# Optimization experiments

Measured on AMD Instinct MI355X. Metric: run time of the kernel, lower is better.

Reference implementation:

```python
import jax, jax.numpy as jnp
import numpy as np

B, N_PIC, C, H, W, P = 32, 4, 3, 224, 224, 16
HP = H // P  # 14
NP = HP * HP  # 196 patches
D = C * P * P  # 768 = hidden_size


def setup_inputs() -> dict:
    key = jax.random.key(0)
    ks = jax.random.split(key, 12)
    s = 0.02
    def lin(k, din, dout):
        kw, kb = jax.random.split(k)
        return (jax.random.normal(kw, (din, dout), jnp.float32) * s,
                jax.random.normal(kb, (dout,), jnp.float32) * s)
    W1, b1 = lin(ks[0], D, D)
    Wq, bq = lin(ks[1], D, D)
    Wk, bk = lin(ks[2], D, D)
    Wv, bv = lin(ks[3], D, D)
    Wo1, bo1 = lin(ks[4], D, D)
    Wo2, bo2 = lin(ks[5], D, D)
    x = jax.random.normal(ks[6], (B, N_PIC, C, H, W), jnp.float32)
    return {"x": x, "W1": W1, "b1": b1, "Wq": Wq, "bq": bq, "Wk": Wk,
            "bk": bk, "Wv": Wv, "bv": bv, "Wo1": Wo1, "bo1": bo1,
            "Wo2": Wo2, "bo2": bo2}


def reference(x, W1, b1, Wq, bq, Wk, bk, Wv, bv, Wo1, bo1, Wo2, bo2):
    b = x.shape[0]
    # patchify: matches torch unfold(3,P,P).unfold(4,P,P) + permute + view
    # -> [b, N, num_patches, C*P*P] with (C, ph, pw) ordering in last dim
    p = x.reshape(b, N_PIC, C, HP, P, HP, P)
    p = p.transpose(0, 1, 3, 5, 2, 4, 6).reshape(b, N_PIC, NP, D)
    h = p @ W1 + b1  # [b, N, S, D]
    # attention: query always from picture 0; key/value per picture (batched)
    Q = h[:, 0] @ Wq + bq          # [b, S, D]
    K = h @ Wk + bk                # [b, N, S, D]
    V = h @ Wv + bv                # [b, N, S, D]
    scale = 1.0 / jnp.sqrt(jnp.float32(D))
    scores = jnp.einsum('bsd,bnmd->bnsm', Q, K) * scale  # [b, N, S, S]
    attn = jax.nn.softmax(scores, axis=-1)
    wv = jnp.einsum('bnsm,bnmd->bnsd', attn, V)           # [b, N, S, D]
    out = jax.nn.relu(wv @ Wo1 + bo1) @ Wo2 + bo2
    return out
```

## Files before the change

kernel.cpp:

```cpp
#include <hip/hip_runtime.h>

typedef __bf16 bf16;
typedef __bf16 bf16x8 __attribute__((ext_vector_type(8)));
typedef float  f32x4  __attribute__((ext_vector_type(4)));


__global__ __launch_bounds__(256) void patchify_k(const float* __restrict__ x,
                                                  bf16* __restrict__ p) {
  int t = blockIdx.x * 256 + threadIdx.x;
  if (t >= 128 * 3 * 14 * 16 * 14) return;
  int j  = t % 14; t /= 14;
  int ph = t % 16; t /= 16;
  int i  = t % 14; t /= 14;
  int c  = t % 3;  t /= 3;
  int bn = t;
  const float* src = x + (((long long)(bn * 3 + c) * 224 + (i * 16 + ph)) * 224 + j * 16);
  bf16* dst = p + ((long long)(bn * 196 + (i * 14 + j)) * 768 + c * 256 + ph * 16);
  bf16 tmp[16];
  for (int k = 0; k < 16; k += 4) {
    float4 f = *(const float4*)(src + k);
    tmp[k + 0] = (bf16)f.x; tmp[k + 1] = (bf16)f.y;
    tmp[k + 2] = (bf16)f.z; tmp[k + 3] = (bf16)f.w;
  }
  *(bf16x8*)(dst)     = *(bf16x8*)&tmp[0];
  *(bf16x8*)(dst + 8) = *(bf16x8*)&tmp[8];
}

__global__ __launch_bounds__(256) void wtrans_k(const float* __restrict__ w0,
                                                const float* __restrict__ w1,
                                                const float* __restrict__ w2,
                                                const float* __restrict__ w3,
                                                const float* __restrict__ w4,
                                                const float* __restrict__ w5,
                                                bf16* __restrict__ out) {
  __shared__ float tile[32][33];
  const float* W;
  switch (blockIdx.z) {
    case 0: W = w0; break; case 1: W = w1; break; case 2: W = w2; break;
    case 3: W = w3; break; case 4: W = w4; break; default: W = w5; break;
  }
  bf16* o = out + (long long)blockIdx.z * 768 * 768;
  int nb = blockIdx.x * 32, kb = blockIdx.y * 32;
  int c = threadIdx.x & 31, r = threadIdx.x >> 5;
  for (int rr = 0; rr < 32; rr += 8)
    tile[r + rr][c] = W[(long long)(kb + r + rr) * 768 + nb + c];
  __syncthreads();
  for (int rr = 0; rr < 32; rr += 8)
    o[(long long)(nb + r + rr) * 768 + kb + c] = (bf16)tile[c][r + rr];
}

__global__ __launch_bounds__(256) void vtrans_k(const bf16* __restrict__ kv,
                                                bf16* __restrict__ Vt) {
  __shared__ short tile[32][33];
  int z = blockIdx.z;
  const short* v = (const short*)(kv + (long long)z * 301056 + 768);
  short* vt = (short*)(Vt + (long long)z * 768 * 224);
  int db = blockIdx.x * 32;
  int mb = blockIdx.y * 32;
  int c = threadIdx.x & 31, r = threadIdx.x >> 5;
  for (int rr = 0; rr < 32; rr += 8) {
    int m = mb + r + rr;
    short val = 0;
    if (m < 196) val = v[(long long)m * 1536 + db + c];
    tile[r + rr][c] = val;
  }
  __syncthreads();
  for (int rr = 0; rr < 32; rr += 8) {
    int d = db + r + rr;
    vt[(long long)d * 224 + mb + c] = tile[c][r + rr];
  }
}

__global__ __launch_bounds__(64) void softmax_k(const float* __restrict__ S,
                                                bf16* __restrict__ attn) {
  const int row = blockIdx.x;
  const float* sr = S + (long long)row * 196;
  const int l = threadIdx.x;
  float v0 = sr[l];
  float v1 = sr[l + 64];
  float v2 = sr[l + 128];
  float v3 = (l + 192 < 196) ? sr[l + 192] : -1e30f;
  float mx = fmaxf(fmaxf(v0, v1), fmaxf(v2, v3));
  for (int o = 32; o > 0; o >>= 1) mx = fmaxf(mx, __shfl_xor(mx, o));
  float e0 = __expf(v0 - mx);
  float e1 = __expf(v1 - mx);
  float e2 = __expf(v2 - mx);
  float e3 = (l + 192 < 196) ? __expf(v3 - mx) : 0.f;
  float s = e0 + e1 + e2 + e3;
  for (int o = 32; o > 0; o >>= 1) s += __shfl_xor(s, o);
  float inv = 1.0f / s;
  bf16* ar = attn + (long long)row * 224;
  ar[l]       = (bf16)(e0 * inv);
  ar[l + 64]  = (bf16)(e1 * inv);
  ar[l + 128] = (bf16)(e2 * inv);
  int m3 = l + 192;
  if (m3 < 196) ar[m3] = (bf16)(e3 * inv);
  else if (m3 < 224) ar[m3] = (bf16)0.0f;
}

__device__ __forceinline__ void gld16(const bf16* g, bf16* l) {
  __builtin_amdgcn_global_load_lds(
      (const __attribute__((address_space(1))) unsigned int*)g,
      (__attribute__((address_space(3))) unsigned int*)l, 16, 0, 0);
}

__global__ __launch_bounds__(256) void gemm128(
    const bf16* __restrict__ A, const bf16* __restrict__ Bt,
    const float* __restrict__ bias, const float* __restrict__ bias2,
    void* __restrict__ Cout,
    int M, int N, int K, int lda, int ldb, int gr, long long gs,
    long long strideAz, int a_zdiv, long long strideBz, long long strideCz,
    float scale, int relu, int out_bf16) {
  __shared__ __align__(16) char smem[34816];
  bf16* AsBuf = (bf16*)smem;
  bf16* BsBuf = (bf16*)(smem + 16384);

  const int tid = threadIdx.x;
  const int lane = tid & 63;
  const int w = tid >> 6;
  const int wm = w & 1, wn = w >> 1;
  const int z = blockIdx.z;
  const int n0 = blockIdx.x * 128, m0 = blockIdx.y * 128;

  const bf16* Az  = A  + (long long)(z / a_zdiv) * strideAz;
  const bf16* Btz = Bt + (long long)z * strideBz;

  const int rl  = 16 * w + (lane & 15);
  const int kc8 = (lane >> 4) * 8;
  int ar0 = m0 + rl;        if (ar0 >= M) ar0 = M - 1;
  int ar1 = m0 + 64 + rl;   if (ar1 >= M) ar1 = M - 1;
  const bf16* aP0 = Az + (long long)(ar0 / gr) * gs + (long long)(ar0 % gr) * lda + kc8;
  const bf16* aP1 = Az + (long long)(ar1 / gr) * gs + (long long)(ar1 % gr) * lda + kc8;
  int br0 = n0 + rl;        if (br0 >= N) br0 = N - 1;
  int br1 = n0 + 64 + rl;   if (br1 >= N) br1 = N - 1;
  const bf16* bP0 = Btz + (long long)br0 * ldb + kc8;
  const bf16* bP1 = Btz + (long long)br1 * ldb + kc8;

  const int dstOff = w * 512;

#define ISSUE(t, buf) do { const int _o = (t) << 5;                 \
    gld16(aP0 + _o, AsBuf + (buf) * 4096 + dstOff);                 \
    gld16(aP1 + _o, AsBuf + (buf) * 4096 + 2048 + dstOff);          \
    gld16(bP0 + _o, BsBuf + (buf) * 4096 + dstOff);                 \
    gld16(bP1 + _o, BsBuf + (buf) * 4096 + 2048 + dstOff); } while (0)

  const int niter = K >> 5;
  f32x4 acc[4][4] = {};
  const int fr = lane & 15, fq = lane >> 4;

  ISSUE(0, 0);

  for (int i = 0; i < niter; ++i) {
    __syncthreads();
    const int cur = i & 1;
    if (i + 1 < niter) ISSUE(i + 1, cur ^ 1);

    const bf16* Ac = AsBuf + cur * 4096;
    const bf16* Bc = BsBuf + cur * 4096;
    bf16x8 a[4], b[4];
#pragma unroll
    for (int mi = 0; mi < 4; mi++)
      a[mi] = *(const bf16x8*)&Ac[(wm * 4 + mi) * 512 + fq * 128 + fr * 8];
#pragma unroll
    for (int ni = 0; ni < 4; ni++)
      b[ni] = *(const bf16x8*)&Bc[(wn * 4 + ni) * 512 + fq * 128 + fr * 8];
#pragma unroll
    for (int mi = 0; mi < 4; mi++)
#pragma unroll
      for (int ni = 0; ni < 4; ni++)
        acc[mi][ni] = __builtin_amdgcn_mfma_f32_16x16x32_bf16(a[mi], b[ni], acc[mi][ni], 0, 0, 0);
  }
#undef ISSUE

  __syncthreads();

  const long long cz = (long long)z * strideCz;
  if (out_bf16) {
    bf16* Cs = (bf16*)smem;
#pragma unroll
    for (int ni = 0; ni < 4; ni++) {
      int col = wn * 64 + ni * 16 + fr;
      int gcol = n0 + col;
      float bb = 0.f;
      if (bias) bb = (bias2 && gcol >= 768) ? bias2[gcol - 768] : bias[gcol];
#pragma unroll
      for (int mi = 0; mi < 4; mi++) {
        int rbase = wm * 64 + mi * 16 + fq * 4;
#pragma unroll
        for (int r = 0; r < 4; r++) {
          float v = acc[mi][ni][r] * scale + bb;
          if (relu) v = fmaxf(v, 0.f);
          Cs[(rbase + r) * 136 + col] = (bf16)v;
        }
      }
    }
    __syncthreads();
    bf16* Cp = (bf16*)Cout;
    const int rr = tid >> 4, cc = (tid & 15) * 8;
#pragma unroll
    for (int pp = 0; pp < 8; pp++) {
      int row = pp * 16 + rr;
      int grow = m0 + row;
      if (grow < M)
        *(bf16x8*)(Cp + cz + (long long)grow * N + n0 + cc) =
            *(const bf16x8*)&Cs[row * 136 + cc];
    }
  } else {
    float* Cs = (float*)smem;
    float* Cp = (float*)Cout;
    for (int half = 0; half < 2; ++half) {
      if (wm == half) {
#pragma unroll
        for (int ni = 0; ni < 4; ni++) {
          int col = wn * 64 + ni * 16 + fr;
          int gcol = n0 + col;
          float bb = 0.f;
          if (bias && gcol < N)
            bb = (bias2 && gcol >= 768) ? bias2[gcol - 768] : bias[gcol];
#pragma unroll
          for (int mi = 0; mi < 4; mi++) {
            int rbase = mi * 16 + fq * 4;
#pragma unroll
            for (int r = 0; r < 4; r++) {
              float v = acc[mi][ni][r] * scale + bb;
              if (relu) v = fmaxf(v, 0.f);
              Cs[(rbase + r) * 132 + col] = v;
            }
          }
        }
      }
      __syncthreads();
      const int rr = tid >> 5, cc = (tid & 31) * 4;
#pragma unroll
      for (int pp = 0; pp < 8; pp++) {
        int row = pp * 8 + rr;
        int grow = m0 + half * 64 + row;
        if (grow < M) {
          int gcol = n0 + cc;
          float* dst = Cp + cz + (long long)grow * N + gcol;
          const float* srcl = &Cs[row * 132 + cc];
          if (gcol + 4 <= N) {
            *(float4*)dst = *(const float4*)srcl;
          } else {
            for (int e = 0; e < 4; e++)
              if (gcol + e < N) dst[e] = srcl[e];
          }
        }
      }
      __syncthreads();
    }
  }
}

__global__ __launch_bounds__(512, 2) void gemm256(
    const bf16* __restrict__ A, const bf16* __restrict__ Bt,
    const float* __restrict__ bias, const float* __restrict__ bias2,
    void* __restrict__ Cout,
    int N, int K, int lda, int ldb, int relu, int out_bf16) {
  __shared__ __align__(16) char smem[131072];
  bf16* As = (bf16*)smem;
  bf16* Bs = (bf16*)(smem + 65536);

  const int tid = threadIdx.x;
  const int lane = tid & 63;
  const int w = tid >> 6;
  const int wm = w >> 2;
  const int wn = w & 3;

  const int nx = N >> 8;
  const int nwg = gridDim.x * gridDim.y;
  int f = blockIdx.y * gridDim.x + blockIdx.x;
  {
    const int q = nwg >> 3, r = nwg & 7;
    const int xcd = f & 7, idx = f >> 3;
    f = (xcd < r ? xcd * (q + 1) : r * (q + 1) + (xcd - r) * q) + idx;
  }
  const int n0 = (f % nx) * 256;
  const int m0 = (f / nx) * 256;

  const int srow = ((tid >> 2) & 15) + ((tid >> 7) << 4);
  const int scol = ((tid >> 6) & 1) * 32 +
                   (((tid & 3) << 3) ^ ((tid & 32) ? 16 : 0));
  const bf16* aBase = A  + (long long)(m0 + srow) * lda + scol;
  const bf16* bBase = Bt + (long long)(n0 + srow) * ldb + scol;
  const int ldsw = w * 512;

#define STG(base, ld, dstArr, buf, kt, hh) do {                              \
    const bf16* _s = (base) + (long long)((hh) * 128) * (ld) + (kt) * 64;    \
    gld16(_s,               (dstArr) + (buf) * 16384 + (hh) * 8192 + ldsw);  \
    gld16(_s + 64LL * (ld), (dstArr) + (buf) * 16384 + (hh) * 8192 + 4096 + ldsw); \
  } while (0)

  const int fr = lane & 15, fq = lane >> 4;
  const int frij = fr * 32 + ((fq * 8) ^ ((fr & 8) ? 16 : 0));
  const bf16* aRd = As + wm * 8192 + frij;
  const bf16* bRd = Bs + (wn >> 1) * 8192 + (wn & 1) * 4096 + frij;

  f32x4 acc[8][4] = {};
  bf16x8 aF[4][2], bF[4][2];

  const int nt = K >> 6;

  STG(aBase, lda, As, 0, 0, 0);
  STG(aBase, lda, As, 0, 0, 1);
  STG(bBase, ldb, Bs, 0, 0, 0);
  STG(bBase, ldb, Bs, 0, 0, 1);
  STG(bBase, ldb, Bs, 1, 1, 0);
  STG(aBase, lda, As, 1, 1, 0);
  asm volatile("s_waitcnt vmcnt(4)" ::: "memory");
  asm volatile("s_barrier" ::: "memory");

  for (int t = 0; t < nt; ++t) {
    const int buf = t & 1;
    const int bOff = buf << 14;

#pragma unroll
    for (int mi = 0; mi < 4; ++mi)
#pragma unroll
      for (int kk = 0; kk < 2; ++kk)
        aF[mi][kk] = *(const bf16x8*)(aRd + bOff + mi * 1024 + kk * 512);
#pragma unroll
    for (int ni = 0; ni < 2; ++ni)
#pragma unroll
      for (int kk = 0; kk < 2; ++kk)
        bF[ni][kk] = *(const bf16x8*)(bRd + bOff + ni * 1024 + kk * 512);
    if (t + 1 < nt) STG(aBase, lda, As, buf ^ 1, t + 1, 1);
    asm volatile("s_barrier" ::: "memory");
    __builtin_amdgcn_s_setprio(1);
#pragma unroll
    for (int mi = 0; mi < 4; ++mi)
#pragma unroll
      for (int ni = 0; ni < 2; ++ni)
#pragma unroll
        for (int kk = 0; kk < 2; ++kk)
          acc[mi][ni] = __builtin_amdgcn_mfma_f32_16x16x32_bf16(
              aF[mi][kk], bF[ni][kk], acc[mi][ni], 0, 0, 0);
    __builtin_amdgcn_s_setprio(0);
    asm volatile("s_barrier" ::: "memory");

#pragma unroll
    for (int ni = 2; ni < 4; ++ni)
#pragma unroll
      for (int kk = 0; kk < 2; ++kk)
        bF[ni][kk] = *(const bf16x8*)(bRd + bOff + ni * 1024 + kk * 512);
    if (t + 1 < nt) STG(bBase, ldb, Bs, buf ^ 1, t + 1, 1);
    asm volatile("s_barrier" ::: "memory");
    __builtin_amdgcn_s_setprio(1);
#pragma unroll
    for (int mi = 0; mi < 4; ++mi)
#pragma unroll
      for (int ni = 2; ni < 4; ++ni)
#pragma unroll
        for (int kk = 0; kk < 2; ++kk)
          acc[mi][ni] = __builtin_amdgcn_mfma_f32_16x16x32_bf16(
              aF[mi][kk], bF[ni][kk], acc[mi][ni], 0, 0, 0);
    __builtin_amdgcn_s_setprio(0);
    asm volatile("s_barrier" ::: "memory");

#pragma unroll
    for (int mi = 0; mi < 4; ++mi)
#pragma unroll
      for (int kk = 0; kk < 2; ++kk)
        aF[mi][kk] = *(const bf16x8*)(aRd + bOff + (4 + mi) * 1024 + kk * 512);
    if (t + 2 < nt) STG(bBase, ldb, Bs, buf, t + 2, 0);
    asm volatile("s_barrier" ::: "memory");
    __builtin_amdgcn_s_setprio(1);
#pragma unroll
    for (int mi = 0; mi < 4; ++mi)
#pragma unroll
      for (int ni = 0; ni < 2; ++ni)
#pragma unroll
        for (int kk = 0; kk < 2; ++kk)
          acc[4 + mi][ni] = __builtin_amdgcn_mfma_f32_16x16x32_bf16(
              aF[mi][kk], bF[ni][kk], acc[4 + mi][ni], 0, 0, 0);
    __builtin_amdgcn_s_setprio(0);
    asm volatile("s_barrier" ::: "memory");

    if (t + 2 < nt) STG(aBase, lda, As, buf, t + 2, 0);
    asm volatile("s_barrier" ::: "memory");
    __builtin_amdgcn_s_setprio(1);
#pragma unroll
    for (int mi = 0; mi < 4; ++mi)
#pragma unroll
      for (int ni = 2; ni < 4; ++ni)
#pragma unroll
        for (int kk = 0; kk < 2; ++kk)
          acc[4 + mi][ni] = __builtin_amdgcn_mfma_f32_16x16x32_bf16(
              aF[mi][kk], bF[ni][kk], acc[4 + mi][ni], 0, 0, 0);
    __builtin_amdgcn_s_setprio(0);
    if (t < nt - 2)       asm volatile("s_waitcnt vmcnt(4)" ::: "memory");
    else if (t == nt - 2) asm volatile("s_waitcnt vmcnt(0)" ::: "memory");
    asm volatile("s_barrier" ::: "memory");
  }
#undef STG

  const long long Nll = N;
  if (out_bf16) {
    bf16* Cs = (bf16*)smem;
    bf16* Cp = (bf16*)Cout;
#pragma unroll
    for (int half = 0; half < 2; ++half) {
      if (wm == half) {
#pragma unroll
        for (int ni = 0; ni < 4; ++ni) {
          const int col = wn * 64 + ni * 16 + fr;
          const int gcol = n0 + col;
          float bb = 0.f;
          if (bias) bb = (bias2 && gcol >= 768) ? bias2[gcol - 768] : bias[gcol];
#pragma unroll
          for (int mi = 0; mi < 8; ++mi) {
#pragma unroll
            for (int r = 0; r < 4; ++r) {
              float v = acc[mi][ni][r] + bb;
              if (relu) v = fmaxf(v, 0.f);
              Cs[(mi * 16 + fq * 4 + r) * 268 + col] = (bf16)v;
            }
          }
        }
      }
      __syncthreads();
      const int row = tid >> 2, cb = (tid & 3) * 8;
      const bf16* srcl = &Cs[row * 268 + cb];
      bf16* dst = Cp + (long long)(m0 + half * 128 + row) * Nll + n0 + cb;
#pragma unroll
      for (int j = 0; j < 8; ++j)
        *(bf16x8*)(dst + j * 32) = *(const bf16x8*)(srcl + j * 32);
      __syncthreads();
    }
  } else {
    float* Cs = (float*)smem;
    float* Cp = (float*)Cout;
#pragma unroll
    for (int pass = 0; pass < 4; ++pass) {
      if (wm == (pass >> 1)) {
#pragma unroll
        for (int ni = 0; ni < 4; ++ni) {
          const int col = wn * 64 + ni * 16 + fr;
          const int gcol = n0 + col;
          float bb = 0.f;
          if (bias) bb = (bias2 && gcol >= 768) ? bias2[gcol - 768] : bias[gcol];
#pragma unroll
          for (int mi2 = 0; mi2 < 4; ++mi2) {
            const int mi = (pass & 1) * 4 + mi2;
#pragma unroll
            for (int r = 0; r < 4; ++r) {
              float v = acc[mi][ni][r] + bb;
              if (relu) v = fmaxf(v, 0.f);
              Cs[(mi2 * 16 + fq * 4 + r) * 268 + col] = v;
            }
          }
        }
      }
      __syncthreads();
      const int row = tid >> 3, c4 = (tid & 7) * 4;
      const float* srcl = &Cs[row * 268 + c4];
      float* dst = Cp + (long long)(m0 + pass * 64 + row) * Nll + n0 + c4;
#pragma unroll
      for (int j = 0; j < 8; ++j)
        *(float4*)(dst + j * 32) = *(const float4*)(srcl + j * 32);
      __syncthreads();
    }
  }
}

extern "C" void kernel_launch(void* const* d_in, const int* in_sizes, int n_in,
                              void* d_out, int out_size, void* d_ws, size_t ws_size,
                              hipStream_t stream) {
  (void)in_sizes; (void)n_in; (void)out_size; (void)ws_size;
  const float* x   = (const float*)d_in[0];
  const float* W1  = (const float*)d_in[1];
  const float* b1  = (const float*)d_in[2];
  const float* Wq  = (const float*)d_in[3];
  const float* bq  = (const float*)d_in[4];
  const float* Wk  = (const float*)d_in[5];
  const float* bk  = (const float*)d_in[6];
  const float* Wv  = (const float*)d_in[7];
  const float* bv  = (const float*)d_in[8];
  const float* Wo1 = (const float*)d_in[9];
  const float* bo1 = (const float*)d_in[10];
  const float* Wo2 = (const float*)d_in[11];
  const float* bo2 = (const float*)d_in[12];

  char* ws = (char*)d_ws;
  bf16*  p    = (bf16*)(ws + 0);
  bf16*  vt   = (bf16*)(ws + 0);
  bf16*  h    = (bf16*)(ws + 44040192LL);
  bf16*  wv   = (bf16*)(ws + 44040192LL);
  bf16*  kv   = (bf16*)(ws + 82575360LL);
  bf16*  o1   = (bf16*)(ws + 82575360LL);
  float* sc   = (float*)(ws + 159645696LL);
  bf16*  q    = (bf16*)(ws + 179314688LL);
  bf16*  attn = (bf16*)(ws + 179314688LL);
  bf16*  wt   = (bf16*)(ws + 190554112LL);
  constexpr long long WSZ = 768LL * 768;

  const float qk_scale = 0.03608439182435161f;

  patchify_k<<<4704, 256, 0, stream>>>(x, p);
  wtrans_k<<<dim3(24, 24, 6), 256, 0, stream>>>(W1, Wk, Wv, Wq, Wo1, Wo2, wt);

  gemm256<<<dim3(3, 98), 512, 0, stream>>>(p, wt + 0 * WSZ, b1, nullptr, h,
      768, 768, 768, 768, 0, 1);
  gemm256<<<dim3(6, 98), 512, 0, stream>>>(h, wt + 1 * WSZ, bk, bv, kv,
      1536, 768, 768, 768, 0, 1);
  gemm128<<<dim3(6, 49, 1), 256, 0, stream>>>(h, wt + 3 * WSZ, bq, nullptr, q,
      6272, 768, 768, 768, 768, 196, 602112LL, 0LL, 1, 0LL, 0LL, 1.f, 0, 1);
  vtrans_k<<<dim3(24, 7, 128), 256, 0, stream>>>(kv, vt);
  gemm128<<<dim3(2, 2, 128), 256, 0, stream>>>(q, kv, nullptr, nullptr, sc,
      196, 196, 768, 768, 1536, 196, 0LL, 150528LL, 4, 301056LL, 38416LL,
      qk_scale, 0, 0);
  softmax_k<<<25088, 64, 0, stream>>>(sc, attn);
  gemm128<<<dim3(6, 2, 128), 256, 0, stream>>>(attn, vt, nullptr, nullptr, wv,
      196, 768, 224, 224, 224, 196, 0LL, 43904LL, 1, 172032LL, 150528LL,
      1.f, 0, 1);
  gemm256<<<dim3(3, 98), 512, 0, stream>>>(wv, wt + 4 * WSZ, bo1, nullptr, o1,
      768, 768, 768, 768, 1, 1);
  gemm256<<<dim3(3, 98), 512, 0, stream>>>(o1, wt + 5 * WSZ, bo2, nullptr,
      (float*)d_out, 768, 768, 768, 768, 0, 0);
}
```

Baseline: 557.6 us.

## Restructure GEMM main loop with register double-buffered fragments and reordered global prefetch

Splits the A/B fragment registers into separate halves so the next tile's A0/B0 fragments are loaded from LDS during the current tile's later MFMA phases, and issues global-to-LDS loads per quarter tile with a new schedule and wait counts. The aim is to overlap LDS reads with MFMA work and hide global load latency better in the 256x256 bf16 GEMM. It uses more registers for fragments, which could lower occupancy or cause spills, and the changed vmcnt and barrier placement carries a risk of ordering mistakes.

```diff
diff --git a/kernel.cpp b/kernel.cpp
--- a/kernel.cpp
+++ b/kernel.cpp
@@ -285,11 +285,9 @@
   const bf16* bBase = Bt + (long long)(n0 + srow) * ldb + scol;
   const int ldsw = w * 512;
 
-#define STG(base, ld, dstArr, buf, kt, hh) do {                              \
-    const bf16* _s = (base) + (long long)((hh) * 128) * (ld) + (kt) * 64;    \
-    gld16(_s,               (dstArr) + (buf) * 16384 + (hh) * 8192 + ldsw);  \
-    gld16(_s + 64LL * (ld), (dstArr) + (buf) * 16384 + (hh) * 8192 + 4096 + ldsw); \
-  } while (0)
+#define STGQ(base, ld, dstArr, buf, kt, hh, q)                               \
+  gld16((base) + (long long)((hh) * 128 + (q) * 64) * (ld) + (kt) * 64,      \
+        (dstArr) + (buf) * 16384 + (hh) * 8192 + (q) * 4096 + ldsw)
 
   const int fr = lane & 15, fq = lane >> 4;
   const int frij = fr * 32 + ((fq * 8) ^ ((fr & 8) ? 16 : 0));
@@ -297,34 +295,52 @@
   const bf16* bRd = Bs + (wn >> 1) * 8192 + (wn & 1) * 4096 + frij;
 
   f32x4 acc[8][4] = {};
-  bf16x8 aF[4][2], bF[4][2];
+  bf16x8 A0f[4][2], A1f[4][2], B0f[2][2], B1f[2][2];
 
   const int nt = K >> 6;
 
-  STG(aBase, lda, As, 0, 0, 0);
-  STG(aBase, lda, As, 0, 0, 1);
-  STG(bBase, ldb, Bs, 0, 0, 0);
-  STG(bBase, ldb, Bs, 0, 0, 1);
-  STG(bBase, ldb, Bs, 1, 1, 0);
-  STG(aBase, lda, As, 1, 1, 0);
-  asm volatile("s_waitcnt vmcnt(4)" ::: "memory");
+  STGQ(aBase, lda, As, 0, 0, 0, 0); STGQ(aBase, lda, As, 0, 0, 1, 0);
+  STGQ(aBase, lda, As, 0, 0, 0, 1); STGQ(aBase, lda, As, 0, 0, 1, 1);
+  STGQ(bBase, ldb, Bs, 0, 0, 0, 0); STGQ(bBase, ldb, Bs, 0, 0, 0, 1);
+  STGQ(bBase, ldb, Bs, 0, 0, 1, 0); STGQ(bBase, ldb, Bs, 0, 0, 1, 1);
+  if (nt > 1) {
+    STGQ(aBase, lda, As, 1, 1, 0, 0); STGQ(aBase, lda, As, 1, 1, 1, 0);
+    STGQ(bBase, ldb, Bs, 1, 1, 0, 0); STGQ(bBase, ldb, Bs, 1, 1, 0, 1);
+    STGQ(bBase, ldb, Bs, 1, 1, 1, 0); STGQ(bBase, ldb, Bs, 1, 1, 1, 1);
+    STGQ(aBase, lda, As, 1, 1, 0, 1); STGQ(aBase, lda, As, 1, 1, 1, 1);
+  }
+  asm volatile("s_waitcnt vmcnt(0)" ::: "memory");
   asm volatile("s_barrier" ::: "memory");
+#pragma unroll
+  for (int mi = 0; mi < 4; ++mi)
+#pragma unroll
+    for (int kk = 0; kk < 2; ++kk)
+      A0f[mi][kk] = *(const bf16x8*)(aRd + mi * 1024 + kk * 512);
+#pragma unroll
+  for (int ni = 0; ni < 2; ++ni)
+#pragma unroll
+    for (int kk = 0; kk < 2; ++kk)
+      B0f[ni][kk] = *(const bf16x8*)(bRd + ni * 1024 + kk * 512);
+  asm volatile("s_waitcnt lgkmcnt(0)" ::: "memory");
+  asm volatile("s_barrier" ::: "memory");
 
   for (int t = 0; t < nt; ++t) {
-    const int buf = t & 1;
-    const int bOff = buf << 14;
-
-#pragma unroll
-    for (int mi = 0; mi < 4; ++mi)
+    const int bo = (t & 1) << 14;
+    const int bn = ((t & 1) ^ 1) << 14;
+    const int b = t & 1;
+
+#pragma unroll
+    for (int ni = 0; ni < 2; ++ni)
 #pragma unroll
       for (int kk = 0; kk < 2; ++kk)
-        aF[mi][kk] = *(const bf16x8*)(aRd + bOff + mi * 1024 + kk * 512);
-#pragma unroll
-    for (int ni = 0; ni < 2; ++ni)
-#pragma unroll
-      for (int kk = 0; kk < 2; ++kk)
-        bF[ni][kk] = *(const bf16x8*)(bRd + bOff + ni * 1024 + kk * 512);
-    if (t + 1 < nt) STG(aBase, lda, As, buf ^ 1, t + 1, 1);
+        B1f[ni][kk] = *(const bf16x8*)(bRd + bo + (2 + ni) * 1024 + kk * 512);
+    if (t + 2 < nt) {
+      STGQ(aBase, lda, As, b, t + 2, 0, 0);
+      STGQ(aBase, lda, As, b, t + 2, 1, 0);
+      asm volatile("s_waitcnt vmcnt(2)" ::: "memory");
+    } else {
+      asm volatile("s_waitcnt vmcnt(0)" ::: "memory");
+    }
     asm volatile("s_barrier" ::: "memory");
     __builtin_amdgcn_s_setprio(1);
 #pragma unroll
@@ -334,35 +350,41 @@
 #pragma unroll
         for (int kk = 0; kk < 2; ++kk)
           acc[mi][ni] = __builtin_amdgcn_mfma_f32_16x16x32_bf16(
-              aF[mi][kk], bF[ni][kk], acc[mi][ni], 0, 0, 0);
+              A0f[mi][kk], B0f[ni][kk], acc[mi][ni], 0, 0, 0);
     __builtin_amdgcn_s_setprio(0);
     asm volatile("s_barrier" ::: "memory");
 
 #pragma unroll
-    for (int ni = 2; ni < 4; ++ni)
+    for (int mi = 0; mi < 4; ++mi)
 #pragma unroll
       for (int kk = 0; kk < 2; ++kk)
-        bF[ni][kk] = *(const bf16x8*)(bRd + bOff + ni * 1024 + kk * 512);
-    if (t + 1 < nt) STG(bBase, ldb, Bs, buf ^ 1, t + 1, 1);
+        A1f[mi][kk] = *(const bf16x8*)(aRd + bo + (4 + mi) * 1024 + kk * 512);
     asm volatile("s_barrier" ::: "memory");
     __builtin_amdgcn_s_setprio(1);
 #pragma unroll
     for (int mi = 0; mi < 4; ++mi)
 #pragma unroll
-      for (int ni = 2; ni < 4; ++ni)
+      for (int ni = 0; ni < 2; ++ni)
 #pragma unroll
         for (int kk = 0; kk < 2; ++kk)
-          acc[mi][ni] = __builtin_amdgcn_mfma_f32_16x16x32_bf16(
-              aF[mi][kk], bF[ni][kk], acc[mi][ni], 0, 0, 0);
+          acc[mi][2 + ni] = __builtin_amdgcn_mfma_f32_16x16x32_bf16(
+              A0f[mi][kk], B1f[ni][kk], acc[mi][2 + ni], 0, 0, 0);
     __builtin_amdgcn_s_setprio(0);
     asm volatile("s_barrier" ::: "memory");
 
-#pragma unroll
-    for (int mi = 0; mi < 4; ++mi)
-#pragma unroll
-      for (int kk = 0; kk < 2; ++kk)
-        aF[mi][kk] = *(const bf16x8*)(aRd + bOff + (4 + mi) * 1024 + kk * 512);
-    if (t + 2 < nt) STG(bBase, ldb, Bs, buf, t + 2, 0);
+    if (t + 1 < nt) {
+#pragma unroll
+      for (int mi = 0; mi < 4; ++mi)
+#pragma unroll
+        for (int kk = 0; kk < 2; ++kk)
+          A0f[mi][kk] = *(const bf16x8*)(aRd + bn + mi * 1024 + kk * 512);
+    }
+    if (t + 2 < nt) {
+      STGQ(bBase, ldb, Bs, b, t + 2, 0, 0);
+      STGQ(bBase, ldb, Bs, b, t + 2, 0, 1);
+      STGQ(bBase, ldb, Bs, b, t + 2, 1, 0);
+      STGQ(bBase, ldb, Bs, b, t + 2, 1, 1);
+    }
     asm volatile("s_barrier" ::: "memory");
     __builtin_amdgcn_s_setprio(1);
 #pragma unroll
@@ -372,27 +394,35 @@
 #pragma unroll
         for (int kk = 0; kk < 2; ++kk)
           acc[4 + mi][ni] = __builtin_amdgcn_mfma_f32_16x16x32_bf16(
-              aF[mi][kk], bF[ni][kk], acc[4 + mi][ni], 0, 0, 0);
+              A1f[mi][kk], B0f[ni][kk], acc[4 + mi][ni], 0, 0, 0);
     __builtin_amdgcn_s_setprio(0);
     asm volatile("s_barrier" ::: "memory");
 
-    if (t + 2 < nt) STG(aBase, lda, As, buf, t + 2, 0);
+    if (t + 1 < nt) {
+#pragma unroll
+      for (int ni = 0; ni < 2; ++ni)
+#pragma unroll
+        for (int kk = 0; kk < 2; ++kk)
+          B0f[ni][kk] = *(const bf16x8*)(bRd + bn + ni * 1024 + kk * 512);
+    }
+    if (t + 2 < nt) {
+      STGQ(aBase, lda, As, b, t + 2, 0, 1);
+      STGQ(aBase, lda, As, b, t + 2, 1, 1);
+    }
     asm volatile("s_barrier" ::: "memory");
     __builtin_amdgcn_s_setprio(1);
 #pragma unroll
     for (int mi = 0; mi < 4; ++mi)
 #pragma unroll
-      for (int ni = 2; ni < 4; ++ni)
+      for (int ni = 0; ni < 2; ++ni)
 #pragma unroll
         for (int kk = 0; kk < 2; ++kk)
-          acc[4 + mi][ni] = __builtin_amdgcn_mfma_f32_16x16x32_bf16(
-              aF[mi][kk], bF[ni][kk], acc[4 + mi][ni], 0, 0, 0);
+          acc[4 + mi][2 + ni] = __builtin_amdgcn_mfma_f32_16x16x32_bf16(
+              A1f[mi][kk], B1f[ni][kk], acc[4 + mi][2 + ni], 0, 0, 0);
     __builtin_amdgcn_s_setprio(0);
-    if (t < nt - 2)       asm volatile("s_waitcnt vmcnt(4)" ::: "memory");
-    else if (t == nt - 2) asm volatile("s_waitcnt vmcnt(0)" ::: "memory");
-    asm volatile("s_barrier" ::: "memory");
-  }
-#undef STG
+    asm volatile("s_barrier" ::: "memory");
+  }
+#undef STGQ
 
   const long long Nll = N;
   if (out_bf16) {
```

Result: no change. 561.3 us (+0.7%).
